# Kernel tuning notes

Measured on AMD Instinct MI355X. Metric: run time of the kernel, lower is better.

The kernel has to match this reference:

```python
import jax, jax.numpy as jnp
import numpy as np

WIDTH = 64
KER_WIDTH = 1024
DEPTH = 6
KER_IN = 6
IN_WIDTH = 1
N_NODES = 10000
N_EDGES = 100000


def setup_inputs() -> dict:
    key = jax.random.key(0)
    ks = jax.random.split(key, 16)
    s = lambda fan_in: 1.0 / np.sqrt(fan_in)
    inp = {
        "x": jax.random.normal(ks[0], (N_NODES, IN_WIDTH), dtype=jnp.float32),
        "edge_index": jax.random.randint(ks[1], (2, N_EDGES), 0, N_NODES, dtype=jnp.int64),
        "edge_attr": jax.random.uniform(ks[2], (N_EDGES, KER_IN), dtype=jnp.float32),
        # fc1
        "fc1_w": jax.random.uniform(ks[3], (IN_WIDTH, WIDTH), jnp.float32, -s(IN_WIDTH), s(IN_WIDTH)),
        "fc1_b": jax.random.uniform(ks[4], (WIDTH,), jnp.float32, -s(IN_WIDTH), s(IN_WIDTH)),
        # kernel DenseNet [KER_IN, 1024, 1024, WIDTH**2]
        "k1_w": jax.random.uniform(ks[5], (KER_IN, KER_WIDTH), jnp.float32, -s(KER_IN), s(KER_IN)),
        "k1_b": jax.random.uniform(ks[6], (KER_WIDTH,), jnp.float32, -s(KER_IN), s(KER_IN)),
        "k2_w": jax.random.uniform(ks[7], (KER_WIDTH, KER_WIDTH), jnp.float32, -s(KER_WIDTH), s(KER_WIDTH)),
        "k2_b": jax.random.uniform(ks[8], (KER_WIDTH,), jnp.float32, -s(KER_WIDTH), s(KER_WIDTH)),
        "k3_w": jax.random.uniform(ks[9], (KER_WIDTH, WIDTH * WIDTH), jnp.float32, -s(KER_WIDTH), s(KER_WIDTH)),
        "k3_b": jax.random.uniform(ks[10], (WIDTH * WIDTH,), jnp.float32, -s(KER_WIDTH), s(KER_WIDTH)),
        # NNConv root weight + bias
        "root": jax.random.uniform(ks[11], (WIDTH, WIDTH), jnp.float32, -s(WIDTH), s(WIDTH)),
        "conv_b": jax.random.uniform(ks[12], (WIDTH,), jnp.float32, -s(WIDTH), s(WIDTH)),
        # fc2
        "fc2_w": jax.random.uniform(ks[13], (WIDTH, 1), jnp.float32, -s(WIDTH), s(WIDTH)),
        "fc2_b": jax.random.uniform(ks[14], (1,), jnp.float32, -s(WIDTH), s(WIDTH)),
    }
    return inp


def reference(x, edge_index, edge_attr, fc1_w, fc1_b, k1_w, k1_b, k2_w, k2_b,
              k3_w, k3_b, root, conv_b, fc2_w, fc2_b):
    n = x.shape[0]
    src, dst = edge_index[0], edge_index[1]  # message flows j (src) -> i (dst)

    # Per-edge kernel MLP -> [E, WIDTH, WIDTH]; edge_attr and kernel weights are
    # identical across the 6 layers, so compute once (same math as recomputing).
    e = jax.nn.relu(edge_attr @ k1_w + k1_b)
    e = jax.nn.relu(e @ k2_w + k2_b)
    W_edge = (e @ k3_w + k3_b).reshape(-1, WIDTH, WIDTH)  # [E, in, out]

    # mean aggregation: divide by in-degree (isolated nodes -> 0, as scatter_mean)
    deg = jax.ops.segment_sum(jnp.ones_like(dst, dtype=x.dtype), dst, num_segments=n)
    inv_deg = jnp.where(deg > 0, 1.0 / deg, 0.0)[:, None]  # [N,1]

    h = x @ fc1_w + fc1_b  # [N, WIDTH]
    for k in range(DEPTH):
        msg = jnp.einsum('ec,eco->eo', h[src], W_edge)              # gather + per-edge matmul
        agg = jax.ops.segment_sum(msg, dst, num_segments=n) * inv_deg  # scatter-mean
        h = agg + h @ root + conv_b
        if k != DEPTH - 1:
            h = jax.nn.relu(h)
    return h @ fc2_w + fc2_b
```

## Files before the change

### kernel.cpp

```cpp
#include <hip/hip_runtime.h>
#include <hip/hip_bf16.h>

#define WIDTH 64
#define KW 1024
#define DEPTH 6
#define NN 10000
#define NE 100000
#define E_PAD 100096
#define MT_ALL (E_PAD / 128)
#define GNODES 32
#define MAXSETS 12
#define NGRP2 313
#define NN_PAD (NGRP2 * GNODES)
#define G1E 16

typedef __attribute__((ext_vector_type(8))) short bf16x8;
typedef __attribute__((ext_vector_type(4))) float f32x4;

#define AS1 __attribute__((address_space(1)))
#define AS3 __attribute__((address_space(3)))

__device__ __forceinline__ float bf2f(unsigned short u) {
  union { unsigned int i; float f; } v; v.i = ((unsigned int)u) << 16; return v.f;
}
__device__ __forceinline__ unsigned short f2bf(float f) {
  union { float f; unsigned int i; } v; v.f = f;
  return (unsigned short)((v.i + 0x7FFFu + ((v.i >> 16) & 1u)) >> 16);
}

__device__ __forceinline__ void gl_lds16(const void* g, void* lds_base) {
#if __has_builtin(__builtin_amdgcn_global_load_lds)
  __builtin_amdgcn_global_load_lds((const AS1 unsigned int*)g,
                                   (AS3 unsigned int*)lds_base, 16, 0, 0);
#else
  *(uint4*)((char*)lds_base + (threadIdx.x & 63) * 16) = *(const uint4*)g;
#endif
}

__global__ void convert_transpose_kernel(const float* __restrict__ in,
                                         unsigned short* __restrict__ out,
                                         int K, int N) {
  long long idx = (long long)blockIdx.x * blockDim.x + threadIdx.x;
  if (idx >= (long long)K * N) return;
  int k = (int)(idx % K);
  int n = (int)(idx / K);
  out[idx] = f2bf(in[(long long)k * N + n]);
}

__global__ void build_kpt3_kernel(const float* __restrict__ k3w,
                                  unsigned short* __restrict__ kp3) {
  int idx = blockIdx.x * blockDim.x + threadIdx.x;
  if (idx >= (64 << 16)) return;
  int o = idx & 63;
  int c = (idx >> 6) & 63;
  int r = idx >> 12;
  int rt = r >> 5, hh = (r >> 4) & 1, l15r = r & 15;
  int chalf = c >> 5, lane_hi = (c >> 3) & 3, j = c & 7;
  int lane = lane_hi * 16 + l15r;
  kp3[(size_t)((((o * 32 + rt) * 2 + hh) * 2 + chalf) * 512) + lane * 8 + j] =
      f2bf(k3w[idx]);
}

__global__ void gemm1_kernel(const float* __restrict__ ea, const float* __restrict__ k1w,
                             const float* __restrict__ k1b, const int* __restrict__ sid,
                             unsigned short* __restrict__ e1c, int e0, int E) {
  __shared__ float af[G1E][6];
  int t = threadIdx.x;
  int p0 = e0 + blockIdx.x * G1E;
  if (t < G1E * 6) {
    int le = t / 6, j = t - le * 6;
    int p = p0 + le;
    int e = (p < E) ? (sid ? sid[p] : p) : -1;
    af[le][j] = (e >= 0) ? ea[(long long)e * 6 + j] : 0.0f;
  }
  __syncthreads();
  int c4 = t * 4;
  float4 b4 = *(const float4*)&k1b[c4];
  float4 w[6];
#pragma unroll
  for (int j = 0; j < 6; j++) w[j] = *(const float4*)&k1w[j * KW + c4];
#pragma unroll 4
  for (int le = 0; le < G1E; le++) {
    float a0 = b4.x, a1 = b4.y, a2 = b4.z, a3 = b4.w;
#pragma unroll
    for (int j = 0; j < 6; j++) {
      float av = af[le][j];
      a0 += av * w[j].x; a1 += av * w[j].y; a2 += av * w[j].z; a3 += av * w[j].w;
    }
    ushort4 o;
    o.x = f2bf(fmaxf(a0, 0.f)); o.y = f2bf(fmaxf(a1, 0.f));
    o.z = f2bf(fmaxf(a2, 0.f)); o.w = f2bf(fmaxf(a3, 0.f));
    *(ushort4*)&e1c[(long long)(blockIdx.x * G1E + le) * KW + c4] = o;
  }
}

__global__ __launch_bounds__(256, 2)
void gemm_bt_kernel(const unsigned short* __restrict__ A,
                    const unsigned short* __restrict__ BT,
                    const float* __restrict__ bias,
                    unsigned short* __restrict__ C,
                    int row0, int N, int K, int mtiles, int do_relu, int kblocked) {
  __shared__ unsigned short sA[128 * 64];
  __shared__ unsigned short sB[128 * 64];
  const int tid  = threadIdx.x;
  const int wave = tid >> 6;
  const int lane = tid & 63;
  const int mt = blockIdx.x % mtiles;
  const int nt = blockIdx.x / mtiles;
  const long long m0 = (long long)mt * 128;
  const int n0 = nt * 128;
  const int wm = wave >> 1, wn = wave & 1;
  const int l15 = lane & 15, quad = lane >> 4;

  f32x4 acc[4][4];
#pragma unroll
  for (int i = 0; i < 4; i++)
#pragma unroll
    for (int j = 0; j < 4; j++) { f32x4 z = {0.f, 0.f, 0.f, 0.f}; acc[i][j] = z; }

  int a_off[4][2], b_off[4][2];
#pragma unroll
  for (int i = 0; i < 4; i++) {
    int ra = wm * 64 + i * 16 + l15;
    int rb = wn * 64 + i * 16 + l15;
#pragma unroll
    for (int kk = 0; kk < 2; kk++) {
      int q = kk * 4 + quad;
      a_off[i][kk] = (ra * 8 + (q ^ (ra & 7))) * 16;
      b_off[i][kk] = (rb * 8 + (q ^ (rb & 7))) * 16;
    }
  }

  int st_row[4], st_q[4];
#pragma unroll
  for (int t = 0; t < 4; t++) {
    int p = (wave * 4 + t) * 64 + lane;
    st_row[t] = p >> 3;
    st_q[t] = (p & 7) ^ ((p >> 3) & 7);
  }

  for (int k0 = 0; k0 < K; k0 += 64) {
    __syncthreads();
#pragma unroll
    for (int t = 0; t < 4; t++) {
      const unsigned short* ga = A + (m0 + st_row[t]) * K + (k0 + st_q[t] * 8);
      const unsigned short* gb = BT + ((long long)(n0 + st_row[t])) * K + (k0 + st_q[t] * 8);
      gl_lds16(ga, (void*)&sA[(wave * 4 + t) * 64 * 8]);
      gl_lds16(gb, (void*)&sB[(wave * 4 + t) * 64 * 8]);
    }
    __syncthreads();

#pragma unroll
    for (int kk = 0; kk < 2; kk++) {
      bf16x8 af[4], bfr[4];
#pragma unroll
      for (int i = 0; i < 4; i++) af[i]  = *(const bf16x8*)((const char*)sA + a_off[i][kk]);
#pragma unroll
      for (int i = 0; i < 4; i++) bfr[i] = *(const bf16x8*)((const char*)sB + b_off[i][kk]);
#pragma unroll
      for (int mi = 0; mi < 4; mi++)
#pragma unroll
        for (int ni = 0; ni < 4; ni++)
          acc[mi][ni] = __builtin_amdgcn_mfma_f32_16x16x32_bf16(af[mi], bfr[ni], acc[mi][ni], 0, 0, 0);
    }
  }

  float bias_v[4];
#pragma unroll
  for (int ni = 0; ni < 4; ni++) bias_v[ni] = bias[n0 + wn * 64 + ni * 16 + l15];
#pragma unroll
  for (int mi = 0; mi < 4; mi++) {
#pragma unroll
    for (int ni = 0; ni < 4; ni++) {
#pragma unroll
      for (int r = 0; r < 4; r++) {
        long long m = m0 + wm * 64 + mi * 16 + quad * 4 + r;
        int n = n0 + wn * 64 + ni * 16 + l15;
        float v = acc[mi][ni][r] + bias_v[ni];
        if (do_relu) v = fmaxf(v, 0.f);
        if (kblocked)
          C[((long long)(n >> 5) * E_PAD + (row0 + m)) * 32 + (n & 31)] = f2bf(v);
        else
          C[m * N + n] = f2bf(v);
      }
    }
  }
}

__global__ void deg_kernel(const int* __restrict__ dst, float* __restrict__ deg, int E) {
  int e = blockIdx.x * blockDim.x + threadIdx.x;
  if (e < E) atomicAdd(&deg[dst[e]], 1.0f);
}

__global__ void count_kernel(const int* __restrict__ key, int* __restrict__ cnt, int E) {
  int e = blockIdx.x * blockDim.x + threadIdx.x;
  if (e < E) atomicAdd(&cnt[key[e]], 1);
}

__global__ void scan_kernel(const int* __restrict__ cnt, int* __restrict__ start,
                            int* __restrict__ cursor) {
  __shared__ int psum[1024];
  int t = threadIdx.x;
  int s0 = t * 10;
  int vals[10];
  int local = 0;
#pragma unroll
  for (int i = 0; i < 10; i++) {
    int idx = s0 + i;
    vals[i] = (idx < NN) ? cnt[idx] : 0;
    local += vals[i];
  }
  psum[t] = local;
  __syncthreads();
  for (int off = 1; off < 1024; off <<= 1) {
    int v = (t >= off) ? psum[t - off] : 0;
    __syncthreads();
    psum[t] += v;
    __syncthreads();
  }
  int excl = psum[t] - local;
#pragma unroll
  for (int i = 0; i < 10; i++) {
    int idx = s0 + i;
    if (idx < NN) { start[idx] = excl; cursor[idx] = excl; excl += vals[i]; }
  }
  if (t == 0) start[NN] = NE;
}

__global__ void scatter_kernel(const int* __restrict__ src, int* __restrict__ cursor,
                               int* __restrict__ sorted_eid, int* __restrict__ pose, int E) {
  int e = blockIdx.x * blockDim.x + threadIdx.x;
  if (e < E) {
    int pos = atomicAdd(&cursor[src[e]], 1);
    sorted_eid[pos] = e;
    pose[e] = pos;
  }
}

__global__ void scatter2_kernel(const int* __restrict__ dst, int* __restrict__ cursor2,
                                const int* __restrict__ pose, int* __restrict__ sid2, int E) {
  int e = blockIdx.x * blockDim.x + threadIdx.x;
  if (e < E) {
    int pos = atomicAdd(&cursor2[dst[e]], 1);
    sid2[pos] = pose[e];
  }
}

__global__ void build_tiles_kernel(const int* __restrict__ start, int2* __restrict__ tiles) {
  int g = blockIdx.x * blockDim.x + threadIdx.x;
  if (g >= NGRP2) return;
  int nt[4] = {0, 0, 0, 0};
  for (int w = 0; w < 4; w++)
    for (int s = 0; s < MAXSETS; s++)
      tiles[(g * 4 + w) * MAXSETS + s] = make_int2(0, 0);
  int t = 0;
  for (int i = 0; i < GNODES; i++) {
    int na = g * GNODES + i;
    int nb = na + 1;
    if (na > NN) na = NN;
    if (nb > NN) nb = NN;
    int s = start[na], e = start[nb];
    for (int m0 = s; m0 < e; m0 += 16) {
      int w = t & 3;
      if (nt[w] < MAXSETS) {
        int c = e - m0; if (c > 16) c = 16;
        tiles[(g * 4 + w) * MAXSETS + nt[w]] = make_int2(i | (c << 16), m0);
        nt[w]++;
      }
      t++;
    }
  }
}

__global__ void h0_mb_kernel(const float* __restrict__ x, const float* __restrict__ fc1w,
                             const float* __restrict__ fc1b, const float* __restrict__ k3b,
                             float* __restrict__ h, unsigned short* __restrict__ hbf,
                             float* __restrict__ mb) {
  int wave = threadIdx.x >> 6, lane = threadIdx.x & 63;
  int n = blockIdx.x * 4 + wave;
  if (n >= NN) return;
  float v = x[n] * fc1w[lane] + fc1b[lane];
  h[n * 64 + lane] = v;
  hbf[n * 64 + lane] = f2bf(v);
  float mbv = 0.f;
#pragma unroll
  for (int c = 0; c < 64; c++)
    mbv += __shfl(v, c, 64) * k3b[c * 64 + lane];
  mb[n * 64 + lane] = mbv;
}

__global__ __launch_bounds__(256, 3)
void fused_msg_kernel(const unsigned short* __restrict__ hbf,
                      const unsigned short* __restrict__ e2p,
                      const unsigned short* __restrict__ kp3,
                      const int2* __restrict__ tiles,
                      const int* __restrict__ sorted_eid,
                      const int* __restrict__ dst,
                      const float* __restrict__ mb,
                      float* __restrict__ agg,
                      unsigned short* __restrict__ msgh,
                      float* __restrict__ msgf,
                      int msg_mode) {
  __shared__ unsigned short slab[GNODES * 512];
  const int tid = threadIdx.x, wave = tid >> 6, lane = tid & 63;
  const int l15 = lane & 15, quad = lane >> 4;
  const int oh = blockIdx.x & 3;
  const int ng = blockIdx.x >> 2;
  const int n0 = ng * GNODES;

  int s_node[MAXSETS], s_j[MAXSETS], s_cnt[MAXSETS], row_off[MAXSETS];
  const int2* tp = tiles + (ng * 4 + wave) * MAXSETS;
#pragma unroll
  for (int s2 = 0; s2 < MAXSETS; s2++) {
    int2 rec = tp[s2];
    s_node[s2] = rec.x & 0xffff;
    s_cnt[s2]  = rec.x >> 16;
    s_j[s2]    = rec.y;
    int c = s_cnt[s2];
    int sl = (l15 < c) ? l15 : (c > 0 ? c - 1 : 0);
    row_off[s2] = (s_j[s2] + sl) * 32 + quad * 8;
  }

  f32x4 acc[MAXSETS];
#pragma unroll
  for (int s2 = 0; s2 < MAXSETS; s2++) { f32x4 z = {0.f, 0.f, 0.f, 0.f}; acc[s2] = z; }

  bf16x8 pb0[2], pb1[2];
#pragma unroll
  for (int g2 = 0; g2 < 2; g2++) {
    pb0[g2] = *(const bf16x8*)(hbf + (n0 + g2 * 16 + l15) * 64 + quad * 8);
    pb1[g2] = *(const bf16x8*)(hbf + (n0 + g2 * 16 + l15) * 64 + 32 + quad * 8);
  }

  for (int rt = 0; rt < 32; rt++) {
    __syncthreads();
    const unsigned short* e2s = e2p + (size_t)rt * (E_PAD * 32);
    bf16x8 apre[MAXSETS];
#pragma unroll
    for (int s2 = 0; s2 < MAXSETS; s2++) {
      if (s_cnt[s2])
        apre[s2] = *(const bf16x8*)(e2s + row_off[s2]);
    }
#pragma unroll 4
    for (int u = 0; u < 8; u++) {
      int id = wave * 8 + u;
      int o_loc = id >> 1, hh = id & 1;
      int o = oh * 16 + o_loc;
      const unsigned short* blk = kp3 + (size_t)(((o * 32 + rt) * 2 + hh) * 2) * 512;
      bf16x8 a0 = *(const bf16x8*)(blk + lane * 8);
      bf16x8 a1 = *(const bf16x8*)(blk + 512 + lane * 8);
      int chunk_log = o_loc * 4 + hh * 2 + (quad >> 1);
      int phys = chunk_log ^ (l15 & 7);
#pragma unroll
      for (int g2 = 0; g2 < 2; g2++) {
        f32x4 c = {0.f, 0.f, 0.f, 0.f};
        c = __builtin_amdgcn_mfma_f32_16x16x32_bf16(a0, pb0[g2], c, 0, 0, 0);
        c = __builtin_amdgcn_mfma_f32_16x16x32_bf16(a1, pb1[g2], c, 0, 0, 0);
        unsigned int w0 = (unsigned int)f2bf(c[0]) | ((unsigned int)f2bf(c[1]) << 16);
        unsigned int w1 = (unsigned int)f2bf(c[2]) | ((unsigned int)f2bf(c[3]) << 16);
        uint2* p = (uint2*)((char*)slab + (g2 * 16 + l15) * 1024 + phys * 16 + (quad & 1) * 8);
        uint2 w; w.x = w0; w.y = w1;
        *p = w;
      }
    }
    __syncthreads();
#pragma unroll
    for (int s2 = 0; s2 < MAXSETS; s2++) {
      if (s_cnt[s2] == 0) continue;
      int node = s_node[s2];
      const char* nb = (const char*)slab + node * 1024;
      bf16x8 b = *(const bf16x8*)(nb + (((l15 * 4 + quad) ^ (node & 7)) * 16));
      acc[s2] = __builtin_amdgcn_mfma_f32_16x16x32_bf16(apre[s2], b, acc[s2], 0, 0, 0);
    }
  }

#pragma unroll
  for (int s2 = 0; s2 < MAXSETS; s2++) {
    if (s_cnt[s2] == 0) continue;
    float mbv = mb[(n0 + s_node[s2]) * 64 + oh * 16 + l15];
#pragma unroll
    for (int reg = 0; reg < 4; reg++) {
      int mloc = quad * 4 + reg;
      if (mloc < s_cnt[s2]) {
        int p = s_j[s2] + mloc;
        float v = acc[s2][reg] + mbv;
        if (msg_mode == 2) {
          __builtin_nontemporal_store(v, &msgf[p * 64 + oh * 16 + l15]);
        } else if (msg_mode == 1) {
          __builtin_nontemporal_store(f2bf(v), &msgh[p * 64 + oh * 16 + l15]);
        } else {
          int d = dst[sorted_eid[p]];
          atomicAdd(&agg[d * 64 + oh * 16 + l15], v);
        }
      }
    }
  }
}

__global__ void scatter_update_mb_kernel(const unsigned short* __restrict__ msgh,
                                         const float* __restrict__ msgf,
                                         const int* __restrict__ startd,
                                         const int* __restrict__ sid2,
                                         const float* __restrict__ h,
                                         const float* __restrict__ root,
                                         const float* __restrict__ convb,
                                         const float* __restrict__ k3b,
                                         float* __restrict__ hout,
                                         unsigned short* __restrict__ hbf,
                                         float* __restrict__ mb,
                                         int do_relu, int msg_mode) {
  int wave = threadIdx.x >> 6, lane = threadIdx.x & 63;
  int n = blockIdx.x * 4 + wave;
  if (n >= NN) return;
  float hv = h[n * 64 + lane];
  float racc = 0.f;
#pragma unroll
  for (int c = 0; c < 64; c++)
    racc += __shfl(hv, c, 64) * root[c * 64 + lane];
  int js = startd[n], je = startd[n + 1];
  float sum = 0.f;
  if (msg_mode == 2) {
    for (int j = js; j < je; j++) { int p = sid2[j]; sum += msgf[p * 64 + lane]; }
  } else {
    for (int j = js; j < je; j++) { int p = sid2[j]; sum += bf2f(msgh[p * 64 + lane]); }
  }
  float inv = (je > js) ? 1.0f / (float)(je - js) : 0.f;
  float v = sum * inv + racc + convb[lane];
  if (do_relu) v = fmaxf(v, 0.f);
  hout[n * 64 + lane] = v;
  hbf[n * 64 + lane] = f2bf(v);
  float mbv = 0.f;
#pragma unroll
  for (int c = 0; c < 64; c++)
    mbv += __shfl(v, c, 64) * k3b[c * 64 + lane];
  mb[n * 64 + lane] = mbv;
}

__global__ void update_mb_kernel(const float* __restrict__ h, const float* __restrict__ agg,
                                 const float* __restrict__ deg, const float* __restrict__ root,
                                 const float* __restrict__ convb, const float* __restrict__ k3b,
                                 float* __restrict__ hout, unsigned short* __restrict__ hbf,
                                 float* __restrict__ mb, int do_relu) {
  int wave = threadIdx.x >> 6, lane = threadIdx.x & 63;
  int n = blockIdx.x * 4 + wave;
  if (n >= NN) return;
  float hv = h[n * 64 + lane];
  float acc = 0.f;
#pragma unroll
  for (int c = 0; c < 64; c++)
    acc += __shfl(hv, c, 64) * root[c * 64 + lane];
  float dg = deg[n];
  float inv = dg > 0.f ? 1.0f / dg : 0.f;
  float v = agg[n * 64 + lane] * inv + acc + convb[lane];
  if (do_relu) v = fmaxf(v, 0.f);
  hout[n * 64 + lane] = v;
  hbf[n * 64 + lane] = f2bf(v);
  float mbv = 0.f;
#pragma unroll
  for (int c = 0; c < 64; c++)
    mbv += __shfl(v, c, 64) * k3b[c * 64 + lane];
  mb[n * 64 + lane] = mbv;
}

__global__ void h0_kernel(const float* __restrict__ x, const float* __restrict__ fc1w,
                          const float* __restrict__ fc1b, float* __restrict__ h) {
  int idx = blockIdx.x * blockDim.x + threadIdx.x;
  if (idx >= NN * WIDTH) return;
  int n = idx >> 6, w = idx & 63;
  h[idx] = x[n] * fc1w[w] + fc1b[w];
}

__global__ void msg_kernel(const float* __restrict__ h, const unsigned short* __restrict__ Wc,
                           const int* __restrict__ src, const int* __restrict__ dst,
                           float* __restrict__ agg, int e0, int e_end) {
  int wave = threadIdx.x >> 6;
  int lane = threadIdx.x & 63;
  int e = e0 + blockIdx.x * 4 + wave;
  if (e >= e_end) return;
  int s = src[e], d = dst[e];
  float hv = h[s * WIDTH + lane];
  const unsigned short* We = Wc + (long long)(e - e0) * 4096;
  float acc = 0.f;
#pragma unroll
  for (int c = 0; c < 64; c++) {
    float hs = __shfl(hv, c, 64);
    acc += hs * bf2f(We[c * 64 + lane]);
  }
  atomicAdd(&agg[d * WIDTH + lane], acc);
}

__global__ void update_kernel(const float* __restrict__ h, const float* __restrict__ agg,
                              const float* __restrict__ deg, const float* __restrict__ root,
                              const float* __restrict__ convb, float* __restrict__ hout,
                              int do_relu) {
  int wave = threadIdx.x >> 6, lane = threadIdx.x & 63;
  int n = blockIdx.x * 4 + wave;
  if (n >= NN) return;
  float hv = h[n * WIDTH + lane];
  float acc = 0.f;
#pragma unroll
  for (int c = 0; c < 64; c++)
    acc += __shfl(hv, c, 64) * root[c * WIDTH + lane];
  float dg = deg[n];
  float inv = dg > 0.f ? 1.0f / dg : 0.f;
  float v = agg[n * WIDTH + lane] * inv + acc + convb[lane];
  if (do_relu) v = fmaxf(v, 0.f);
  hout[n * WIDTH + lane] = v;
}

__global__ void fc2_kernel(const float* __restrict__ h, const float* __restrict__ fc2w,
                           const float* __restrict__ fc2b, float* __restrict__ out) {
  int wave = threadIdx.x >> 6, lane = threadIdx.x & 63;
  int n = blockIdx.x * 4 + wave;
  if (n >= NN) return;
  float v = h[n * WIDTH + lane] * fc2w[lane];
#pragma unroll
  for (int off = 32; off > 0; off >>= 1) v += __shfl_down(v, off, 64);
  if (lane == 0) out[n] = v + fc2b[0];
}

extern "C" void kernel_launch(void* const* d_in, const int* in_sizes, int n_in,
                              void* d_out, int out_size, void* d_ws, size_t ws_size,
                              hipStream_t stream) {
  const float* x     = (const float*)d_in[0];
  const int*   ei    = (const int*)d_in[1];
  const float* ea    = (const float*)d_in[2];
  const float* fc1w  = (const float*)d_in[3];
  const float* fc1b  = (const float*)d_in[4];
  const float* k1w   = (const float*)d_in[5];
  const float* k1b   = (const float*)d_in[6];
  const float* k2w   = (const float*)d_in[7];
  const float* k2b   = (const float*)d_in[8];
  const float* k3w   = (const float*)d_in[9];
  const float* k3b   = (const float*)d_in[10];
  const float* root  = (const float*)d_in[11];
  const float* convb = (const float*)d_in[12];
  const float* fc2w  = (const float*)d_in[13];
  const float* fc2b  = (const float*)d_in[14];
  float* out = (float*)d_out;
  const int* src = ei;
  const int* dst = ei + NE;

  char* ws = (char*)d_ws;
  size_t off = 0;
  auto alloc = [&](size_t bytes) -> char* {
    char* p = ws + off; off = (off + bytes + 255) & ~(size_t)255; return p;
  };
  auto al = [](size_t x) { return (x + 255) & ~(size_t)255; };

  unsigned short* k2wT = (unsigned short*)alloc((size_t)KW * KW * 2);
  float* ha  = (float*)alloc((size_t)NN * WIDTH * 4);
  float* hb  = (float*)alloc((size_t)NN * WIDTH * 4);
  float* agg = (float*)alloc((size_t)NN * WIDTH * 4);
  float* deg = (float*)alloc((size_t)NN * 4);
  if (ws_size < off + 4096) return;

  const size_t PT_CH = 128 * KW * 2;

  size_t sz_kpt  = (size_t)(64 << 16) * 2;
  size_t sz_mb   = (size_t)NN * 64 * 4;
  size_t sz_hbf  = (size_t)NN_PAD * 64 * 2;
  size_t sz_cnt  = (size_t)NN * 4;
  size_t sz_st   = (size_t)(NN + 1) * 4;
  size_t sz_sid  = (size_t)NE * 4;
  size_t sz_e2   = (size_t)E_PAD * KW * 2;
  size_t sz_tiles = (size_t)NGRP2 * 4 * MAXSETS * 8;

  size_t core = al(sz_kpt) + al(sz_mb) + al(sz_hbf) + al(sz_cnt) + al(sz_st) + al(sz_cnt)
              + al(sz_sid) + al(sz_e2) + al(sz_tiles) + al(sz_sid) ;
  size_t msg_csr = al(sz_cnt) + al(sz_st) + al(sz_cnt) + al(sz_sid);
  size_t e1c_min = al((size_t)8 * PT_CH);

  int msg_mode;
  if (ws_size >= off + core + msg_csr + al((size_t)NE * 64 * 2) + e1c_min)  msg_mode = 1;
  else if (ws_size >= off + core + e1c_min + 8192)                          msg_mode = 0;
  else                                                                      msg_mode = -1;

  if (msg_mode >= 0) {
    unsigned short* kp3 = (unsigned short*)alloc(sz_kpt);
    float* mb   = (float*)alloc(sz_mb);
    unsigned short* hbf = (unsigned short*)alloc(sz_hbf);
    int* cnt    = (int*)alloc(sz_cnt);
    int* starta = (int*)alloc(sz_st);
    int* cursor = (int*)alloc(sz_cnt);
    int* sid    = (int*)alloc(sz_sid);
    unsigned short* e2p = (unsigned short*)alloc(sz_e2);
    int2* tiles = (int2*)alloc(sz_tiles);
    int* pose   = (int*)alloc(sz_sid);
    int* cnt2 = nullptr; int* startd = nullptr;
    int* cursor2 = nullptr; int* sid2 = nullptr;
    unsigned short* msgh = nullptr; float* msgf = nullptr;
    if (msg_mode >= 1) {
      cnt2    = (int*)alloc(sz_cnt);
      startd  = (int*)alloc(sz_st);
      cursor2 = (int*)alloc(sz_cnt);
      sid2    = (int*)alloc(sz_sid);
      msgh    = (unsigned short*)alloc((size_t)NE * 64 * 2);
    }
    size_t left = ws_size - off;
    int TC = (int)(left / PT_CH); if (TC > MT_ALL) TC = MT_ALL;
    unsigned short* e1c = (unsigned short*)alloc((size_t)TC * PT_CH);

    convert_transpose_kernel<<<(KW * KW) / 256, 256, 0, stream>>>(k2w, k2wT, KW, KW);
    build_kpt3_kernel<<<(64 << 16) / 256, 256, 0, stream>>>(k3w, kp3);
    hipMemsetAsync(cnt, 0, sz_cnt, stream);
    count_kernel<<<(NE + 255) / 256, 256, 0, stream>>>(src, cnt, NE);
    scan_kernel<<<1, 1024, 0, stream>>>(cnt, starta, cursor);
    scatter_kernel<<<(NE + 255) / 256, 256, 0, stream>>>(src, cursor, sid, pose, NE);
    build_tiles_kernel<<<(NGRP2 + 255) / 256, 256, 0, stream>>>(starta, tiles);
    if (msg_mode >= 1) {
      hipMemsetAsync(cnt2, 0, sz_cnt, stream);
      count_kernel<<<(NE + 255) / 256, 256, 0, stream>>>(dst, cnt2, NE);
      scan_kernel<<<1, 1024, 0, stream>>>(cnt2, startd, cursor2);
      scatter2_kernel<<<(NE + 255) / 256, 256, 0, stream>>>(dst, cursor2, pose, sid2, NE);
    } else {
      hipMemsetAsync(deg, 0, (size_t)NN * 4, stream);
      deg_kernel<<<(NE + 255) / 256, 256, 0, stream>>>(dst, deg, NE);
    }
    h0_mb_kernel<<<(NN + 3) / 4, 256, 0, stream>>>(x, fc1w, fc1b, k3b, ha, hbf, mb);
    for (int t0 = 0; t0 < MT_ALL; t0 += TC) {
      int tc = (MT_ALL - t0 < TC) ? (MT_ALL - t0) : TC;
      gemm1_kernel<<<tc * 128 / G1E, 256, 0, stream>>>(ea, k1w, k1b, sid, e1c, t0 * 128, NE);
      gemm_bt_kernel<<<tc * (KW / 128), 256, 0, stream>>>(
          e1c, k2wT, k2b, e2p, t0 * 128, KW, KW, tc, 1, 1);
    }
    float* hc = ha; float* hn = hb;
    for (int k = 0; k < DEPTH; k++) {
      if (msg_mode == 0) hipMemsetAsync(agg, 0, (size_t)NN * WIDTH * 4, stream);
      fused_msg_kernel<<<4 * NGRP2, 256, 0, stream>>>(
          hbf, e2p, kp3, tiles, sid, dst, mb, agg, msgh, msgf, msg_mode);
      if (msg_mode >= 1)
        scatter_update_mb_kernel<<<(NN + 3) / 4, 256, 0, stream>>>(
            msgh, msgf, startd, sid2, hc, root, convb, k3b, hn, hbf, mb,
            (k != DEPTH - 1) ? 1 : 0, msg_mode);
      else
        update_mb_kernel<<<(NN + 3) / 4, 256, 0, stream>>>(
            hc, agg, deg, root, convb, k3b, hn, hbf, mb, (k != DEPTH - 1) ? 1 : 0);
      float* t = hc; hc = hn; hn = t;
    }
    fc2_kernel<<<(NN + 3) / 4, 256, 0, stream>>>(hc, fc2w, fc2b, out);
  } else {
    unsigned short* k3wT = (unsigned short*)alloc((size_t)4096 * KW * 2);
    size_t rem = (ws_size > off) ? ws_size - off : 0;
    const size_t PT_W = 128 * 4096 * 2;
    size_t per_tile = 2 * PT_CH + PT_W;
    long long tcl = (long long)(rem / per_tile);
    int TC = (tcl > 98) ? 98 : (int)tcl;
    if (TC < 1) return;
    unsigned short* e1c = (unsigned short*)alloc((size_t)TC * PT_CH);
    unsigned short* e2c = (unsigned short*)alloc((size_t)TC * PT_CH);
    unsigned short* Wc  = (unsigned short*)alloc((size_t)TC * PT_W);

    convert_transpose_kernel<<<(KW * KW) / 256, 256, 0, stream>>>(k2w, k2wT, KW, KW);
    convert_transpose_kernel<<<(KW * 4096) / 256, 256, 0, stream>>>(k3w, k3wT, KW, 4096);
    hipMemsetAsync(deg, 0, (size_t)NN * 4, stream);
    deg_kernel<<<(NE + 255) / 256, 256, 0, stream>>>(dst, deg, NE);
    h0_kernel<<<(NN * WIDTH) / 256, 256, 0, stream>>>(x, fc1w, fc1b, ha);

    float* hc = ha; float* hn = hb;
    for (int k = 0; k < DEPTH; k++) {
      hipMemsetAsync(agg, 0, (size_t)NN * WIDTH * 4, stream);
      for (int t0 = 0; t0 < MT_ALL; t0 += TC) {
        int tc = (MT_ALL - t0 < TC) ? (MT_ALL - t0) : TC;
        gemm1_kernel<<<tc * 128 / G1E, 256, 0, stream>>>(ea, k1w, k1b, nullptr, e1c,
                                                         t0 * 128, NE);
        gemm_bt_kernel<<<tc * (KW / 128), 256, 0, stream>>>(e1c, k2wT, k2b, e2c,
                                                            0, KW, KW, tc, 1, 0);
        gemm_bt_kernel<<<tc * (4096 / 128), 256, 0, stream>>>(e2c, k3wT, k3b, Wc,
                                                              0, 4096, KW, tc, 0, 0);
        int e0 = t0 * 128;
        int e_end = (t0 + tc) * 128; if (e_end > NE) e_end = NE;
        if (e_end > e0)
          msg_kernel<<<(e_end - e0 + 3) / 4, 256, 0, stream>>>(hc, Wc, src, dst, agg, e0, e_end);
      }
      update_kernel<<<(NN + 3) / 4, 256, 0, stream>>>(hc, agg, deg, root, convb, hn,
                                                      (k != DEPTH - 1) ? 1 : 0);
      float* t = hc; hc = hn; hn = t;
    }
    fc2_kernel<<<(NN + 3) / 4, 256, 0, stream>>>(hc, fc2w, fc2b, out);
  }
}
```

Measured before the change: 3.950 ms.

## Fuse node update and mb projection into the start of the message kernel

The separate per-layer scatter/update kernel is folded into the prologue of the fused message kernel. Each block gathers its group's incoming bf16 messages, applies the root matvec, ReLU and k3 bias projection, and writes the bf16 node features straight into shared memory instead of round-tripping them through a global hbf buffer. Messages are double-buffered across layers, and only one final update kernel remains before fc2. This removes a launch and a global write/read per layer, but each node's update is now computed redundantly by the four output-slice blocks. The atomic and fp32 fallback message modes are also dropped.

Result: slower. 7.631 ms (+93.2%).

```diff
diff --git a/kernel.cpp b/kernel.cpp
--- a/kernel.cpp
+++ b/kernel.cpp
@@ -272,41 +272,61 @@
   }
 }
 
-__global__ void h0_mb_kernel(const float* __restrict__ x, const float* __restrict__ fc1w,
-                             const float* __restrict__ fc1b, const float* __restrict__ k3b,
-                             float* __restrict__ h, unsigned short* __restrict__ hbf,
-                             float* __restrict__ mb) {
-  int wave = threadIdx.x >> 6, lane = threadIdx.x & 63;
-  int n = blockIdx.x * 4 + wave;
-  if (n >= NN) return;
-  float v = x[n] * fc1w[lane] + fc1b[lane];
-  h[n * 64 + lane] = v;
-  hbf[n * 64 + lane] = f2bf(v);
-  float mbv = 0.f;
-#pragma unroll
-  for (int c = 0; c < 64; c++)
-    mbv += __shfl(v, c, 64) * k3b[c * 64 + lane];
-  mb[n * 64 + lane] = mbv;
-}
-
 __global__ __launch_bounds__(256, 3)
-void fused_msg_kernel(const unsigned short* __restrict__ hbf,
+void fused_msg_kernel(const float* __restrict__ x,
+                      const float* __restrict__ fc1w,
+                      const float* __restrict__ fc1b,
+                      const float* __restrict__ h_prev,
+                      float* __restrict__ h_out,
+                      const unsigned short* __restrict__ msg_in,
+                      unsigned short* __restrict__ msg_out,
                       const unsigned short* __restrict__ e2p,
                       const unsigned short* __restrict__ kp3,
                       const int2* __restrict__ tiles,
-                      const int* __restrict__ sorted_eid,
-                      const int* __restrict__ dst,
-                      const float* __restrict__ mb,
-                      float* __restrict__ agg,
-                      unsigned short* __restrict__ msgh,
-                      float* __restrict__ msgf,
-                      int msg_mode) {
+                      const int* __restrict__ startd,
+                      const int* __restrict__ sid2,
+                      const float* __restrict__ root,
+                      const float* __restrict__ convb,
+                      const float* __restrict__ k3b,
+                      float* __restrict__ mb,
+                      int depth0) {
   __shared__ unsigned short slab[GNODES * 512];
   const int tid = threadIdx.x, wave = tid >> 6, lane = tid & 63;
   const int l15 = lane & 15, quad = lane >> 4;
   const int oh = blockIdx.x & 3;
   const int ng = blockIdx.x >> 2;
   const int n0 = ng * GNODES;
+
+  {
+    unsigned short* shb = (unsigned short*)slab;
+    for (int u = 0; u < 8; u++) {
+      int node = wave * 8 + u;
+      int n = n0 + node;
+      float v = 0.f;
+      if (n < NN) {
+        if (depth0) {
+          v = x[n] * fc1w[lane] + fc1b[lane];
+        } else {
+          int js = startd[n], je = startd[n + 1];
+          float sum = 0.f;
+          for (int j = js; j < je; j++) sum += bf2f(msg_in[sid2[j] * 64 + lane]);
+          float hv = h_prev[n * 64 + lane];
+          float racc = 0.f;
+#pragma unroll
+          for (int c = 0; c < 64; c++) racc += __shfl(hv, c, 64) * root[c * 64 + lane];
+          float inv = (je > js) ? 1.0f / (float)(je - js) : 0.f;
+          v = fmaxf(sum * inv + racc + convb[lane], 0.f);
+        }
+        h_out[n * 64 + lane] = v;
+        float mbv = 0.f;
+#pragma unroll
+        for (int c = 0; c < 64; c++) mbv += __shfl(v, c, 64) * k3b[c * 64 + lane];
+        mb[n * 64 + lane] = mbv;
+      }
+      shb[node * 64 + lane] = f2bf(v);
+    }
+  }
+  __syncthreads();
 
   int s_node[MAXSETS], s_j[MAXSETS], s_cnt[MAXSETS], row_off[MAXSETS];
   const int2* tp = tiles + (ng * 4 + wave) * MAXSETS;
@@ -328,8 +348,9 @@
   bf16x8 pb0[2], pb1[2];
 #pragma unroll
   for (int g2 = 0; g2 < 2; g2++) {
-    pb0[g2] = *(const bf16x8*)(hbf + (n0 + g2 * 16 + l15) * 64 + quad * 8);
-    pb1[g2] = *(const bf16x8*)(hbf + (n0 + g2 * 16 + l15) * 64 + 32 + quad * 8);
+    const unsigned short* shb = (const unsigned short*)slab;
+    pb0[g2] = *(const bf16x8*)(shb + (g2 * 16 + l15) * 64 + quad * 8);
+    pb1[g2] = *(const bf16x8*)(shb + (g2 * 16 + l15) * 64 + 32 + quad * 8);
   }
 
   for (int rt = 0; rt < 32; rt++) {
@@ -383,32 +404,21 @@
       int mloc = quad * 4 + reg;
       if (mloc < s_cnt[s2]) {
         int p = s_j[s2] + mloc;
-        float v = acc[s2][reg] + mbv;
-        if (msg_mode == 2) {
-          __builtin_nontemporal_store(v, &msgf[p * 64 + oh * 16 + l15]);
-        } else if (msg_mode == 1) {
-          __builtin_nontemporal_store(f2bf(v), &msgh[p * 64 + oh * 16 + l15]);
-        } else {
-          int d = dst[sorted_eid[p]];
-          atomicAdd(&agg[d * 64 + oh * 16 + l15], v);
-        }
+        __builtin_nontemporal_store(f2bf(acc[s2][reg] + mbv),
+                                    &msg_out[p * 64 + oh * 16 + l15]);
       }
     }
   }
 }
 
 __global__ void scatter_update_mb_kernel(const unsigned short* __restrict__ msgh,
-                                         const float* __restrict__ msgf,
                                          const int* __restrict__ startd,
                                          const int* __restrict__ sid2,
                                          const float* __restrict__ h,
                                          const float* __restrict__ root,
                                          const float* __restrict__ convb,
-                                         const float* __restrict__ k3b,
                                          float* __restrict__ hout,
-                                         unsigned short* __restrict__ hbf,
-                                         float* __restrict__ mb,
-                                         int do_relu, int msg_mode) {
+                                         int do_relu) {
   int wave = threadIdx.x >> 6, lane = threadIdx.x & 63;
   int n = blockIdx.x * 4 + wave;
   if (n >= NN) return;
@@ -419,47 +429,11 @@
     racc += __shfl(hv, c, 64) * root[c * 64 + lane];
   int js = startd[n], je = startd[n + 1];
   float sum = 0.f;
-  if (msg_mode == 2) {
-    for (int j = js; j < je; j++) { int p = sid2[j]; sum += msgf[p * 64 + lane]; }
-  } else {
-    for (int j = js; j < je; j++) { int p = sid2[j]; sum += bf2f(msgh[p * 64 + lane]); }
-  }
+  for (int j = js; j < je; j++) { int p = sid2[j]; sum += bf2f(msgh[p * 64 + lane]); }
   float inv = (je > js) ? 1.0f / (float)(je - js) : 0.f;
   float v = sum * inv + racc + convb[lane];
   if (do_relu) v = fmaxf(v, 0.f);
   hout[n * 64 + lane] = v;
-  hbf[n * 64 + lane] = f2bf(v);
-  float mbv = 0.f;
-#pragma unroll
-  for (int c = 0; c < 64; c++)
-    mbv += __shfl(v, c, 64) * k3b[c * 64 + lane];
-  mb[n * 64 + lane] = mbv;
-}
-
-__global__ void update_mb_kernel(const float* __restrict__ h, const float* __restrict__ agg,
-                                 const float* __restrict__ deg, const float* __restrict__ root,
-                                 const float* __restrict__ convb, const float* __restrict__ k3b,
-                                 float* __restrict__ hout, unsigned short* __restrict__ hbf,
-                                 float* __restrict__ mb, int do_relu) {
-  int wave = threadIdx.x >> 6, lane = threadIdx.x & 63;
-  int n = blockIdx.x * 4 + wave;
-  if (n >= NN) return;
-  float hv = h[n * 64 + lane];
-  float acc = 0.f;
-#pragma unroll
-  for (int c = 0; c < 64; c++)
-    acc += __shfl(hv, c, 64) * root[c * 64 + lane];
-  float dg = deg[n];
-  float inv = dg > 0.f ? 1.0f / dg : 0.f;
-  float v = agg[n * 64 + lane] * inv + acc + convb[lane];
-  if (do_relu) v = fmaxf(v, 0.f);
-  hout[n * 64 + lane] = v;
-  hbf[n * 64 + lane] = f2bf(v);
-  float mbv = 0.f;
-#pragma unroll
-  for (int c = 0; c < 64; c++)
-    mbv += __shfl(v, c, 64) * k3b[c * 64 + lane];
-  mb[n * 64 + lane] = mbv;
 }
 
 __global__ void h0_kernel(const float* __restrict__ x, const float* __restrict__ fc1w,
@@ -559,27 +533,22 @@
 
   size_t sz_kpt  = (size_t)(64 << 16) * 2;
   size_t sz_mb   = (size_t)NN * 64 * 4;
-  size_t sz_hbf  = (size_t)NN_PAD * 64 * 2;
   size_t sz_cnt  = (size_t)NN * 4;
   size_t sz_st   = (size_t)(NN + 1) * 4;
   size_t sz_sid  = (size_t)NE * 4;
   size_t sz_e2   = (size_t)E_PAD * KW * 2;
   size_t sz_tiles = (size_t)NGRP2 * 4 * MAXSETS * 8;
-
-  size_t core = al(sz_kpt) + al(sz_mb) + al(sz_hbf) + al(sz_cnt) + al(sz_st) + al(sz_cnt)
-              + al(sz_sid) + al(sz_e2) + al(sz_tiles) + al(sz_sid) ;
-  size_t msg_csr = al(sz_cnt) + al(sz_st) + al(sz_cnt) + al(sz_sid);
+  size_t sz_msg  = (size_t)NE * 64 * 2;
+
+  size_t core = al(sz_kpt) + al(sz_mb) + al(sz_cnt) + al(sz_st) + al(sz_cnt)
+              + al(sz_sid) + al(sz_e2) + al(sz_tiles) + al(sz_sid)
+              + al(sz_cnt) + al(sz_st) + al(sz_cnt) + al(sz_sid)
+              + 2 * al(sz_msg);
   size_t e1c_min = al((size_t)8 * PT_CH);
 
-  int msg_mode;
-  if (ws_size >= off + core + msg_csr + al((size_t)NE * 64 * 2) + e1c_min)  msg_mode = 1;
-  else if (ws_size >= off + core + e1c_min + 8192)                          msg_mode = 0;
-  else                                                                      msg_mode = -1;
-
-  if (msg_mode >= 0) {
+  if (ws_size >= off + core + e1c_min) {
     unsigned short* kp3 = (unsigned short*)alloc(sz_kpt);
     float* mb   = (float*)alloc(sz_mb);
-    unsigned short* hbf = (unsigned short*)alloc(sz_hbf);
     int* cnt    = (int*)alloc(sz_cnt);
     int* starta = (int*)alloc(sz_st);
     int* cursor = (int*)alloc(sz_cnt);
@@ -587,16 +556,12 @@
     unsigned short* e2p = (unsigned short*)alloc(sz_e2);
     int2* tiles = (int2*)alloc(sz_tiles);
     int* pose   = (int*)alloc(sz_sid);
-    int* cnt2 = nullptr; int* startd = nullptr;
-    int* cursor2 = nullptr; int* sid2 = nullptr;
-    unsigned short* msgh = nullptr; float* msgf = nullptr;
-    if (msg_mode >= 1) {
-      cnt2    = (int*)alloc(sz_cnt);
-      startd  = (int*)alloc(sz_st);
-      cursor2 = (int*)alloc(sz_cnt);
-      sid2    = (int*)alloc(sz_sid);
-      msgh    = (unsigned short*)alloc((size_t)NE * 64 * 2);
-    }
+    int* cnt2   = (int*)alloc(sz_cnt);
+    int* startd = (int*)alloc(sz_st);
+    int* cursor2= (int*)alloc(sz_cnt);
+    int* sid2   = (int*)alloc(sz_sid);
+    unsigned short* msg0 = (unsigned short*)alloc(sz_msg);
+    unsigned short* msg1 = (unsigned short*)alloc(sz_msg);
     size_t left = ws_size - off;
     int TC = (int)(left / PT_CH); if (TC > MT_ALL) TC = MT_ALL;
     unsigned short* e1c = (unsigned short*)alloc((size_t)TC * PT_CH);
@@ -608,37 +573,32 @@
     scan_kernel<<<1, 1024, 0, stream>>>(cnt, starta, cursor);
     scatter_kernel<<<(NE + 255) / 256, 256, 0, stream>>>(src, cursor, sid, pose, NE);
     build_tiles_kernel<<<(NGRP2 + 255) / 256, 256, 0, stream>>>(starta, tiles);
-    if (msg_mode >= 1) {
-      hipMemsetAsync(cnt2, 0, sz_cnt, stream);
-      count_kernel<<<(NE + 255) / 256, 256, 0, stream>>>(dst, cnt2, NE);
-      scan_kernel<<<1, 1024, 0, stream>>>(cnt2, startd, cursor2);
-      scatter2_kernel<<<(NE + 255) / 256, 256, 0, stream>>>(dst, cursor2, pose, sid2, NE);
-    } else {
-      hipMemsetAsync(deg, 0, (size_t)NN * 4, stream);
-      deg_kernel<<<(NE + 255) / 256, 256, 0, stream>>>(dst, deg, NE);
-    }
-    h0_mb_kernel<<<(NN + 3) / 4, 256, 0, stream>>>(x, fc1w, fc1b, k3b, ha, hbf, mb);
+    hipMemsetAsync(cnt2, 0, sz_cnt, stream);
+    count_kernel<<<(NE + 255) / 256, 256, 0, stream>>>(dst, cnt2, NE);
+    scan_kernel<<<1, 1024, 0, stream>>>(cnt2, startd, cursor2);
+    scatter2_kernel<<<(NE + 255) / 256, 256, 0, stream>>>(dst, cursor2, pose, sid2, NE);
     for (int t0 = 0; t0 < MT_ALL; t0 += TC) {
       int tc = (MT_ALL - t0 < TC) ? (MT_ALL - t0) : TC;
       gemm1_kernel<<<tc * 128 / G1E, 256, 0, stream>>>(ea, k1w, k1b, sid, e1c, t0 * 128, NE);
       gemm_bt_kernel<<<tc * (KW / 128), 256, 0, stream>>>(
           e1c, k2wT, k2b, e2p, t0 * 128, KW, KW, tc, 1, 1);
     }
-    float* hc = ha; float* hn = hb;
+    float* hbufs[2] = {ha, hb};
+    unsigned short* msgs[2] = {msg0, msg1};
     for (int k = 0; k < DEPTH; k++) {
-      if (msg_mode == 0) hipMemsetAsync(agg, 0, (size_t)NN * WIDTH * 4, stream);
       fused_msg_kernel<<<4 * NGRP2, 256, 0, stream>>>(
-          hbf, e2p, kp3, tiles, sid, dst, mb, agg, msgh, msgf, msg_mode);
-      if (msg_mode >= 1)
-        scatter_update_mb_kernel<<<(NN + 3) / 4, 256, 0, stream>>>(
-            msgh, msgf, startd, sid2, hc, root, convb, k3b, hn, hbf, mb,
-            (k != DEPTH - 1) ? 1 : 0, msg_mode);
-      else
-        update_mb_kernel<<<(NN + 3) / 4, 256, 0, stream>>>(
-            hc, agg, deg, root, convb, k3b, hn, hbf, mb, (k != DEPTH - 1) ? 1 : 0);
-      float* t = hc; hc = hn; hn = t;
-    }
-    fc2_kernel<<<(NN + 3) / 4, 256, 0, stream>>>(hc, fc2w, fc2b, out);
+          x, fc1w, fc1b,
+          (k == 0) ? ha : hbufs[(k - 1) & 1],
+          hbufs[k & 1],
+          (k == 0) ? msg0 : msgs[(k - 1) & 1],
+          msgs[k & 1],
+          e2p, kp3, tiles, startd, sid2, root, convb, k3b, mb,
+          (k == 0) ? 1 : 0);
+    }
+    scatter_update_mb_kernel<<<(NN + 3) / 4, 256, 0, stream>>>(
+        msgs[(DEPTH - 1) & 1], startd, sid2, hbufs[(DEPTH - 1) & 1],
+        root, convb, agg , 0);
+    fc2_kernel<<<(NN + 3) / 4, 256, 0, stream>>>(agg, fc2w, fc2b, out);
   } else {
     unsigned short* k3wT = (unsigned short*)alloc((size_t)4096 * KW * 2);
     size_t rem = (ws_size > off) ? ws_size - off : 0;
```
